# Kernel tuning notes

Hardware: AMD Instinct MI355X
Metric: run time of the kernel (lower is better)

The kernel has to match this reference:

```python
import jax, jax.numpy as jnp
import numpy as np

VOCAB = 30522
H = 100
T, B = 256, 16


def _lstm(x, W_ih, W_hh, b_ih, b_hh):
    # x: [T, B, I]; PyTorch gate order: i, f, g, o stacked in 4H rows.
    gx = jnp.einsum('tbi,gi->tbg', x, W_ih) + b_ih + b_hh  # [T, B, 4H]
    Hd = W_hh.shape[1]
    h0 = jnp.zeros((x.shape[1], Hd), x.dtype)
    c0 = jnp.zeros((x.shape[1], Hd), x.dtype)

    def step(carry, g_t):
        h, c = carry
        gates = g_t + h @ W_hh.T
        i, f, g, o = jnp.split(gates, 4, axis=-1)
        c = jax.nn.sigmoid(f) * c + jax.nn.sigmoid(i) * jnp.tanh(g)
        h = jax.nn.sigmoid(o) * jnp.tanh(c)
        return (h, c), h

    (h, c), hs = jax.lax.scan(step, (h0, c0), gx)
    return hs, (h, c)


def setup_inputs() -> dict:
    key = jax.random.key(0)
    ks = jax.random.split(key, 12)
    s = 1.0 / np.sqrt(H)
    u = lambda k, shp: jax.random.uniform(k, shp, jnp.float32, -s, s)
    return {
        'input': jax.random.randint(ks[0], (T, B), 0, VOCAB),
        'emb': jax.random.normal(ks[1], (VOCAB, H), jnp.float32),
        'enc_W_ih': u(ks[2], (4 * H, H)),
        'enc_W_hh': u(ks[3], (4 * H, H)),
        'enc_b_ih': u(ks[4], (4 * H,)),
        'enc_b_hh': u(ks[5], (4 * H,)),
        'dec_W_ih': u(ks[6], (4 * H, H)),
        'dec_W_hh': u(ks[7], (4 * H, H)),
        'dec_b_ih': u(ks[8], (4 * H,)),
        'dec_b_hh': u(ks[9], (4 * H,)),
        'out_W': u(ks[10], (VOCAB, H)),
        'out_b': u(ks[11], (VOCAB,)),
    }


def reference(input, emb, enc_W_ih, enc_W_hh, enc_b_ih, enc_b_hh,
              dec_W_ih, dec_W_hh, dec_b_ih, dec_b_hh, out_W, out_b):
    embedded = emb[input]  # [T, B, H]
    # Encoder is run in the original forward but its (hidden, cell) are unused.
    _hs, (_h, _c) = _lstm(embedded, enc_W_ih, enc_W_hh, enc_b_ih, enc_b_hh)
    dec_out, _ = _lstm(embedded, dec_W_ih, dec_W_hh, dec_b_ih, dec_b_hh)
    out = jnp.einsum('tbh,vh->tbv', dec_out, out_W) + out_b  # [T, B, VOCAB]
    return out
```

## Files before the change

### kernel.cpp

```cpp
#include <hip/hip_runtime.h>

#define HH 100
#define G4 400
#define TT 256
#define BB 16
#define TB 4096
#define VV 30522
#define VP 30528
#define KP 128
#define GX_ROWS 8

typedef unsigned short u16;
typedef __attribute__((ext_vector_type(8))) short s16x8;
typedef __attribute__((ext_vector_type(4))) float f32x4;

__device__ __forceinline__ u16 f2bf(float x) {
    unsigned u = __float_as_uint(x);
    return (u16)((u + 0x7fffu + ((u >> 16) & 1u)) >> 16);
}
__device__ __forceinline__ float bf2f(u16 h) {
    return __uint_as_float((unsigned)h << 16);
}

__global__ void k_tw_ih(const float* __restrict__ W, float* __restrict__ Wt) {
    int idx = blockIdx.x * blockDim.x + threadIdx.x;
    if (idx < G4 * HH) {
        int j = idx / HH, k = idx - j * HH;
        Wt[k * G4 + j] = W[idx];
    }
}

__global__ __launch_bounds__(256) void k_prep_w(const float* __restrict__ W,
                                                u16* __restrict__ Bh,
                                                u16* __restrict__ Bl) {
    int idx = blockIdx.x * 256 + threadIdx.x;
    int v = idx >> 4;
    int kc = (idx & 15) * 8;
    s16x8 vh, vl;
    #pragma unroll
    for (int j = 0; j < 8; ++j) {
        int k = kc + j;
        float x = (v < VV && k < HH) ? W[(long)v * HH + k] : 0.f;
        u16 hi = f2bf(x);
        vh[j] = (short)hi;
        vl[j] = (short)f2bf(x - bf2f(hi));
    }
    *(s16x8*)(Bh + (long)v * KP + kc) = vh;
    *(s16x8*)(Bl + (long)v * KP + kc) = vl;
}

__global__ __launch_bounds__(256) void k_gx(const int* __restrict__ tok,
                                            const float* __restrict__ emb,
                                            const float* __restrict__ WtIh,
                                            const float* __restrict__ bih,
                                            const float* __restrict__ bhh,
                                            float* __restrict__ gx) {
    __shared__ float x_s[GX_ROWS * HH];
    int tid = threadIdx.x;
    int row0 = blockIdx.x * GX_ROWS;
    for (int i = tid; i < GX_ROWS * HH; i += 256) {
        int r = i / HH, k = i - r * HH;
        x_s[i] = emb[(long)tok[row0 + r] * HH + k];
    }
    __syncthreads();
    for (int j = tid; j < G4; j += 256) {
        float bias = bih[j] + bhh[j];
        float acc[GX_ROWS];
        #pragma unroll
        for (int r = 0; r < GX_ROWS; ++r) acc[r] = bias;
        for (int k = 0; k < HH; ++k) {
            float w = WtIh[k * G4 + j];
            #pragma unroll
            for (int r = 0; r < GX_ROWS; ++r) acc[r] += w * x_s[r * HH + k];
        }
        #pragma unroll
        for (int r = 0; r < GX_ROWS; ++r) gx[(long)(row0 + r) * G4 + j] = acc[r];
    }
}

__global__ __launch_bounds__(512) void k_lstm(const float* __restrict__ gx,
                                              const float* __restrict__ Whh,
                                              u16* __restrict__ Ah,
                                              u16* __restrict__ Al) {
    __shared__ float h_s[HH];
    __shared__ float gates_s[G4];
    int tid = threadIdx.x;
    int b = blockIdx.x;
    float w[HH];
    if (tid < G4) {
        #pragma unroll
        for (int k = 0; k < HH; ++k) w[k] = Whh[tid * HH + k];
    }
    float c = 0.f;
    if (tid < HH) h_s[tid] = 0.f;
    __syncthreads();
    for (int t = 0; t < TT; ++t) {
        int row = t * BB + b;
        if (tid < G4) {
            float gxv = gx[(long)row * G4 + tid];
            float a0 = 0.f, a1 = 0.f, a2 = 0.f, a3 = 0.f;
            #pragma unroll
            for (int k = 0; k < HH; k += 4) {
                a0 += w[k]     * h_s[k];
                a1 += w[k + 1] * h_s[k + 1];
                a2 += w[k + 2] * h_s[k + 2];
                a3 += w[k + 3] * h_s[k + 3];
            }
            gates_s[tid] = gxv + ((a0 + a1) + (a2 + a3));
        }
        __syncthreads();
        if (tid < HH) {
            float gi = gates_s[tid];
            float gf = gates_s[HH + tid];
            float gg = gates_s[2 * HH + tid];
            float go = gates_s[3 * HH + tid];
            float si = 1.f / (1.f + expf(-gi));
            float sf = 1.f / (1.f + expf(-gf));
            float so = 1.f / (1.f + expf(-go));
            float tg = tanhf(gg);
            c = sf * c + si * tg;
            float h = so * tanhf(c);
            h_s[tid] = h;
            u16 hi = f2bf(h);
            Ah[(long)row * KP + tid] = hi;
            Al[(long)row * KP + tid] = f2bf(h - bf2f(hi));
        } else if (tid < KP) {
            Ah[(long)row * KP + tid] = 0;
            Al[(long)row * KP + tid] = 0;
        }
        __syncthreads();
    }
}

__global__ __launch_bounds__(256) void k_proj_mfma(const u16* __restrict__ Ah,
                                                   const u16* __restrict__ Al,
                                                   const u16* __restrict__ Bh,
                                                   const u16* __restrict__ Bl,
                                                   const float* __restrict__ ob,
                                                   float* __restrict__ out) {
    int tid  = threadIdx.x;
    int wid  = tid >> 6;
    int lane = tid & 63;
    int r    = lane & 15;
    int ko   = (lane >> 4) * 8;

    int m0 = blockIdx.y * 64 + (wid >> 1) * 32;
    int n0 = blockIdx.x * 64 + (wid & 1) * 32;

    const u16* pAh = Ah + (long)(m0 + r) * KP + ko;
    const u16* pAl = Al + (long)(m0 + r) * KP + ko;
    const u16* pBh = Bh + (long)(n0 + r) * KP + ko;
    const u16* pBl = Bl + (long)(n0 + r) * KP + ko;

    f32x4 acc00 = {0.f, 0.f, 0.f, 0.f};
    f32x4 acc01 = {0.f, 0.f, 0.f, 0.f};
    f32x4 acc10 = {0.f, 0.f, 0.f, 0.f};
    f32x4 acc11 = {0.f, 0.f, 0.f, 0.f};

    #pragma unroll
    for (int ks = 0; ks < 4; ++ks) {
        int off = ks * 32;
        s16x8 ah0 = *(const s16x8*)(pAh + off);
        s16x8 ah1 = *(const s16x8*)(pAh + off + 16 * KP);
        s16x8 al0 = *(const s16x8*)(pAl + off);
        s16x8 al1 = *(const s16x8*)(pAl + off + 16 * KP);
        s16x8 bh0 = *(const s16x8*)(pBh + off);
        s16x8 bh1 = *(const s16x8*)(pBh + off + 16 * KP);
        s16x8 bl0 = *(const s16x8*)(pBl + off);
        s16x8 bl1 = *(const s16x8*)(pBl + off + 16 * KP);
#define MM(d, a, b) d = __builtin_amdgcn_mfma_f32_16x16x32_bf16(a, b, d, 0, 0, 0)
        MM(acc00, ah0, bh0); MM(acc00, ah0, bl0); MM(acc00, al0, bh0);
        MM(acc01, ah0, bh1); MM(acc01, ah0, bl1); MM(acc01, al0, bh1);
        MM(acc10, ah1, bh0); MM(acc10, ah1, bl0); MM(acc10, al1, bh0);
        MM(acc11, ah1, bh1); MM(acc11, ah1, bl1); MM(acc11, al1, bh1);
#undef MM
    }

    int hi4 = (lane >> 4) * 4;
    int n_0 = n0 + r;
    int n_1 = n0 + 16 + r;
    bool ok0 = n_0 < VV;
    bool ok1 = n_1 < VV;
    float bias0 = ok0 ? ob[n_0] : 0.f;
    float bias1 = ok1 ? ob[n_1] : 0.f;
    long base0 = (long)(m0 + hi4) * VV;
    long base1 = (long)(m0 + 16 + hi4) * VV;

    if (ok0) {
        #pragma unroll
        for (int q = 0; q < 4; ++q) out[base0 + (long)q * VV + n_0] = acc00[q] + bias0;
        #pragma unroll
        for (int q = 0; q < 4; ++q) out[base1 + (long)q * VV + n_0] = acc10[q] + bias0;
    }
    if (ok1) {
        #pragma unroll
        for (int q = 0; q < 4; ++q) out[base0 + (long)q * VV + n_1] = acc01[q] + bias1;
        #pragma unroll
        for (int q = 0; q < 4; ++q) out[base1 + (long)q * VV + n_1] = acc11[q] + bias1;
    }
}

extern "C" void kernel_launch(void* const* d_in, const int* in_sizes, int n_in,
                              void* d_out, int out_size, void* d_ws, size_t ws_size,
                              hipStream_t stream) {
    const int*   tok  = (const int*)d_in[0];
    const float* emb  = (const float*)d_in[1];
    const float* dWih = (const float*)d_in[6];
    const float* dWhh = (const float*)d_in[7];
    const float* dbih = (const float*)d_in[8];
    const float* dbhh = (const float*)d_in[9];
    const float* outW = (const float*)d_in[10];
    const float* outb = (const float*)d_in[11];
    float* out = (float*)d_out;

    u16* Ah = (u16*)d_ws;
    u16* Al = Ah + (long)TB * KP;
    float* WtIh = (float*)(Al + (long)TB * KP);
    char* big = (char*)(WtIh + (long)HH * G4);
    float* gx = (float*)big;
    u16* Bh = (u16*)big;
    u16* Bl = Bh + (long)VP * KP;

    k_tw_ih<<<(G4 * HH + 255) / 256, 256, 0, stream>>>(dWih, WtIh);
    k_gx<<<TB / GX_ROWS, 256, 0, stream>>>(tok, emb, WtIh, dbih, dbhh, gx);
    k_lstm<<<BB, 512, 0, stream>>>(gx, dWhh, Ah, Al);
    k_prep_w<<<(VP * 16) / 256, 256, 0, stream>>>(outW, Bh, Bl);
    k_proj_mfma<<<dim3(VP / 64, TB / 64), 256, 0, stream>>>(Ah, Al, Bh, Bl, outb, out);
}
```

Measured before the change: 1.325 ms.

## Use MFMA for LSTM recurrence, XCD-aware projection tiling, nontemporal output stores

The recurrent h@W_hh^T matvec in the LSTM kernel now runs on bf16 MFMA using a hi/lo split (three products) instead of per-thread scalar FMAs over 100 registers. Weights are kept as MFMA fragments in registers and h is shared in LDS as bf16 hi/lo. The projection kernel switches to a 1D grid remapped so each XCD handles a contiguous range of vocabulary tiles, with VP padded to 30720. Output writes use nontemporal stores. The split-bf16 recurrence trades a little accuracy for shorter serial step latency.

```diff
diff --git a/kernel.cpp b/kernel.cpp
--- a/kernel.cpp
+++ b/kernel.cpp
@@ -6,7 +6,7 @@
 #define BB 16
 #define TB 4096
 #define VV 30522
-#define VP 30528
+#define VP 30720
 #define KP 128
 #define GX_ROWS 8
 
@@ -21,6 +21,8 @@
 __device__ __forceinline__ float bf2f(u16 h) {
     return __uint_as_float((unsigned)h << 16);
 }
+
+#define MM(d, a, b) d = __builtin_amdgcn_mfma_f32_16x16x32_bf16(a, b, d, 0, 0, 0)
 
 __global__ void k_tw_ih(const float* __restrict__ W, float* __restrict__ Wt) {
     int idx = blockIdx.x * blockDim.x + threadIdx.x;
@@ -82,48 +84,106 @@
                                               const float* __restrict__ Whh,
                                               u16* __restrict__ Ah,
                                               u16* __restrict__ Al) {
-    __shared__ float h_s[HH];
-    __shared__ float gates_s[G4];
+    __shared__ __align__(16) float gmv[G4];
+    __shared__ __align__(16) u16 hhi[KP];
+    __shared__ __align__(16) u16 hlo[KP];
     int tid = threadIdx.x;
+    int w = tid >> 6, l = tid & 63;
     int b = blockIdx.x;
-    float w[HH];
-    if (tid < G4) {
-        #pragma unroll
-        for (int k = 0; k < HH; ++k) w[k] = Whh[tid * HH + k];
-    }
-    float c = 0.f;
-    if (tid < HH) h_s[tid] = 0.f;
+    int r = l & 15;
+    int ks8 = (l >> 4) * 8;
+
+    int mts[4];
+    int ntile = 0;
+    for (int mt = w; mt < 25; mt += 8) mts[ntile++] = mt;
+    s16x8 Afh[4][4], Afl[4][4];
+    #pragma unroll
+    for (int i = 0; i < 4; ++i) {
+        #pragma unroll
+        for (int kt = 0; kt < 4; ++kt) {
+            s16x8 vh = {0,0,0,0,0,0,0,0}, vl = {0,0,0,0,0,0,0,0};
+            if (i < ntile) {
+                int row = mts[i] * 16 + r;
+                int k0 = kt * 32 + ks8;
+                #pragma unroll
+                for (int j = 0; j < 8; ++j) {
+                    int k = k0 + j;
+                    float x = (k < HH) ? Whh[row * HH + k] : 0.f;
+                    u16 hi = f2bf(x);
+                    vh[j] = (short)hi;
+                    vl[j] = (short)f2bf(x - bf2f(hi));
+                }
+            }
+            Afh[i][kt] = vh;
+            Afl[i][kt] = vl;
+        }
+    }
+
+    float c_reg = 0.f;
+    if (tid < KP) { hhi[tid] = 0; hlo[tid] = 0; }
     __syncthreads();
+
     for (int t = 0; t < TT; ++t) {
         int row = t * BB + b;
-        if (tid < G4) {
-            float gxv = gx[(long)row * G4 + tid];
-            float a0 = 0.f, a1 = 0.f, a2 = 0.f, a3 = 0.f;
+        s16x8 Bh_[4], Bl_[4];
+        #pragma unroll
+        for (int kt = 0; kt < 4; ++kt) {
+            Bh_[kt] = *(const s16x8*)&hhi[kt * 32 + ks8];
+            Bl_[kt] = *(const s16x8*)&hlo[kt * 32 + ks8];
+        }
+        float gxv0 = 0.f, gxv1 = 0.f, gxv2 = 0.f, gxv3 = 0.f;
+        if (tid < HH) {
+            const float* gxr = gx + (long)row * G4 + tid;
+            gxv0 = gxr[0];
+            gxv1 = gxr[HH];
+            gxv2 = gxr[2 * HH];
+            gxv3 = gxr[3 * HH];
+        }
+        f32x4 aH[4], aM[4], aL[4];
+        #pragma unroll
+        for (int i = 0; i < 4; ++i) {
+            aH[i] = f32x4{0.f, 0.f, 0.f, 0.f};
+            aM[i] = f32x4{0.f, 0.f, 0.f, 0.f};
+            aL[i] = f32x4{0.f, 0.f, 0.f, 0.f};
+        }
+        #pragma unroll
+        for (int i = 0; i < 4; ++i) {
+            if (i < ntile) {
+                #pragma unroll
+                for (int kt = 0; kt < 4; ++kt) {
+                    MM(aH[i], Afh[i][kt], Bh_[kt]);
+                    MM(aM[i], Afh[i][kt], Bl_[kt]);
+                    MM(aL[i], Afl[i][kt], Bh_[kt]);
+                }
+            }
+        }
+        if (r == 0) {
             #pragma unroll
-            for (int k = 0; k < HH; k += 4) {
-                a0 += w[k]     * h_s[k];
-                a1 += w[k + 1] * h_s[k + 1];
-                a2 += w[k + 2] * h_s[k + 2];
-                a3 += w[k + 3] * h_s[k + 3];
+            for (int i = 0; i < 4; ++i) {
+                if (i < ntile) {
+                    f32x4 s = aH[i] + aM[i] + aL[i];
+                    *(f32x4*)&gmv[mts[i] * 16 + (l >> 4) * 4] = s;
+                }
             }
-            gates_s[tid] = gxv + ((a0 + a1) + (a2 + a3));
         }
         __syncthreads();
         if (tid < HH) {
-            float gi = gates_s[tid];
-            float gf = gates_s[HH + tid];
-            float gg = gates_s[2 * HH + tid];
-            float go = gates_s[3 * HH + tid];
+            float gi = gmv[tid]          + gxv0;
+            float gf = gmv[HH + tid]     + gxv1;
+            float gg = gmv[2 * HH + tid] + gxv2;
+            float go = gmv[3 * HH + tid] + gxv3;
             float si = 1.f / (1.f + expf(-gi));
             float sf = 1.f / (1.f + expf(-gf));
             float so = 1.f / (1.f + expf(-go));
             float tg = tanhf(gg);
-            c = sf * c + si * tg;
-            float h = so * tanhf(c);
-            h_s[tid] = h;
+            c_reg = sf * c_reg + si * tg;
+            float h = so * tanhf(c_reg);
             u16 hi = f2bf(h);
+            u16 lo = f2bf(h - bf2f(hi));
+            hhi[tid] = hi;
+            hlo[tid] = lo;
             Ah[(long)row * KP + tid] = hi;
-            Al[(long)row * KP + tid] = f2bf(h - bf2f(hi));
+            Al[(long)row * KP + tid] = lo;
         } else if (tid < KP) {
             Ah[(long)row * KP + tid] = 0;
             Al[(long)row * KP + tid] = 0;
@@ -144,8 +204,14 @@
     int r    = lane & 15;
     int ko   = (lane >> 4) * 8;
 
-    int m0 = blockIdx.y * 64 + (wid >> 1) * 32;
-    int n0 = blockIdx.x * 64 + (wid & 1) * 32;
+    int id  = blockIdx.x;
+    int xcd = id & 7;
+    int j   = id >> 3;
+    int nt  = xcd * 60 + (j % 60);
+    int mt  = j / 60;
+
+    int m0 = mt * 64 + (wid >> 1) * 32;
+    int n0 = nt * 64 + (wid & 1) * 32;
 
     const u16* pAh = Ah + (long)(m0 + r) * KP + ko;
     const u16* pAl = Al + (long)(m0 + r) * KP + ko;
@@ -168,12 +234,10 @@
         s16x8 bh1 = *(const s16x8*)(pBh + off + 16 * KP);
         s16x8 bl0 = *(const s16x8*)(pBl + off);
         s16x8 bl1 = *(const s16x8*)(pBl + off + 16 * KP);
-#define MM(d, a, b) d = __builtin_amdgcn_mfma_f32_16x16x32_bf16(a, b, d, 0, 0, 0)
         MM(acc00, ah0, bh0); MM(acc00, ah0, bl0); MM(acc00, al0, bh0);
         MM(acc01, ah0, bh1); MM(acc01, ah0, bl1); MM(acc01, al0, bh1);
         MM(acc10, ah1, bh0); MM(acc10, ah1, bl0); MM(acc10, al1, bh0);
         MM(acc11, ah1, bh1); MM(acc11, ah1, bl1); MM(acc11, al1, bh1);
-#undef MM
     }
 
     int hi4 = (lane >> 4) * 4;
@@ -186,17 +250,15 @@
     long base0 = (long)(m0 + hi4) * VV;
     long base1 = (long)(m0 + 16 + hi4) * VV;
 
-    if (ok0) {
-        #pragma unroll
-        for (int q = 0; q < 4; ++q) out[base0 + (long)q * VV + n_0] = acc00[q] + bias0;
-        #pragma unroll
-        for (int q = 0; q < 4; ++q) out[base1 + (long)q * VV + n_0] = acc10[q] + bias0;
-    }
-    if (ok1) {
-        #pragma unroll
-        for (int q = 0; q < 4; ++q) out[base0 + (long)q * VV + n_1] = acc01[q] + bias1;
-        #pragma unroll
-        for (int q = 0; q < 4; ++q) out[base1 + (long)q * VV + n_1] = acc11[q] + bias1;
+    #pragma unroll
+    for (int q = 0; q < 4; ++q) {
+        if (ok0) __builtin_nontemporal_store(acc00[q] + bias0, &out[base0 + (long)q * VV + n_0]);
+        if (ok1) __builtin_nontemporal_store(acc01[q] + bias1, &out[base0 + (long)q * VV + n_1]);
+    }
+    #pragma unroll
+    for (int q = 0; q < 4; ++q) {
+        if (ok0) __builtin_nontemporal_store(acc10[q] + bias0, &out[base1 + (long)q * VV + n_0]);
+        if (ok1) __builtin_nontemporal_store(acc11[q] + bias1, &out[base1 + (long)q * VV + n_1]);
     }
 }
 
@@ -225,5 +287,5 @@
     k_gx<<<TB / GX_ROWS, 256, 0, stream>>>(tok, emb, WtIh, dbih, dbhh, gx);
     k_lstm<<<BB, 512, 0, stream>>>(gx, dWhh, Ah, Al);
     k_prep_w<<<(VP * 16) / 256, 256, 0, stream>>>(outW, Bh, Bl);
-    k_proj_mfma<<<dim3(VP / 64, TB / 64), 256, 0, stream>>>(Ah, Al, Bh, Bl, outb, out);
-}
+    k_proj_mfma<<<VP / 64 * (TB / 64), 256, 0, stream>>>(Ah, Al, Bh, Bl, outb, out);
+}
```

Measured after the change: 1.318 ms. Within noise of the previous version (-0.5%).
